# Performance work log

Hardware: AMD Instinct MI355X
Metric: run time of the kernel (lower is better)

Reference implementation:

```python
import jax, jax.numpy as jnp
import numpy as np

N_NODES = 50000
N_EDGES = 800000
IN_DIM = 3
OUT_DIM = 50


def _glorot(key, shape):
    fan_in, fan_out = shape[0], shape[1]
    lim = np.sqrt(6.0 / (fan_in + fan_out))
    return jax.random.uniform(key, shape, jnp.float32, -lim, lim)


def setup_inputs() -> dict:
    key = jax.random.key(0)
    ks = jax.random.split(key, 16)
    x = jax.random.normal(ks[0], (N_NODES, IN_DIM), jnp.float32)
    edge_index = jax.random.randint(ks[1], (2, N_EDGES), 0, N_NODES, jnp.int64)
    return {
        "x": x,
        "edge_index": edge_index,
        # pointwise Conv1d (kernel_size=1) == per-node Linear; store as [in, out]
        "w1": _glorot(ks[2], (IN_DIM, 32)), "b1": jnp.zeros((32,), jnp.float32),
        "w2": _glorot(ks[3], (32, 64)),     "b2": jnp.zeros((64,), jnp.float32),
        "w3": _glorot(ks[4], (64, 128)),    "b3": jnp.zeros((128,), jnp.float32),
        # GCNConv weights [in, out] + bias
        "g1w": _glorot(ks[5], (128, 256)),  "g1b": jnp.zeros((256,), jnp.float32),
        "g2w": _glorot(ks[6], (256, 512)),  "g2b": jnp.zeros((512,), jnp.float32),
        "g3w": _glorot(ks[7], (512, OUT_DIM)), "g3b": jnp.zeros((OUT_DIM,), jnp.float32),
    }


def _gcn_conv(h, src, dst, dinv, W, b):
    """PyG GCNConv: add self-loops + symmetric norm. h: [N, Fin]."""
    n = h.shape[0]
    h = h @ W  # [N, Fout]
    norm = dinv[src] * dinv[dst]  # [E]
    msg = h[src] * norm[:, None]  # gather over edges [E, Fout]
    agg = jax.ops.segment_sum(msg, dst, num_segments=n)
    # self-loop contribution: norm = dinv[i]^2
    agg = agg + h * (dinv * dinv)[:, None]
    return agg + b


def reference(x, edge_index, w1, b1, w2, b2, w3, b3, g1w, g1b, g2w, g2b, g3w, g3b):
    src, dst = edge_index[0], edge_index[1]
    n = x.shape[0]
    # degree with self-loops (in-degree on targets), shared by all GCN layers
    deg = jnp.zeros((n,), x.dtype).at[dst].add(1.0) + 1.0
    dinv = jax.lax.rsqrt(deg)

    # pointwise conv stack (1x1 Conv1d == per-node dense layer)
    h = jax.nn.relu(x @ w1 + b1)
    h = jax.nn.relu(h @ w2 + b2)
    h = jax.nn.relu(h @ w3 + b3)

    h = jax.nn.relu(_gcn_conv(h, src, dst, dinv, g1w, g1b))
    h = jax.nn.relu(_gcn_conv(h, src, dst, dinv, g2w, g2b))
    h = _gcn_conv(h, src, dst, dinv, g3w, g3b)
    return jax.nn.softmax(h, axis=1)  # [N, OUT_DIM]
```

## Files before the change

kernel.cpp:

```cpp
#include <hip/hip_runtime.h>
#include <hip/hip_bf16.h>
#include <math.h>


typedef __attribute__((ext_vector_type(8))) short short8;
typedef __attribute__((ext_vector_type(8))) _Float16 half8;
typedef __attribute__((ext_vector_type(4))) float floatx4;

__device__ __forceinline__ unsigned short bf16h(float f) {
    unsigned int u = __float_as_uint(f);
    u += 0x7fff + ((u >> 16) & 1);
    return (unsigned short)(u >> 16);
}
__device__ __forceinline__ float bf16f(unsigned short h) {
    return __uint_as_float(((unsigned int)h) << 16);
}

__device__ __forceinline__ void gld_lds16(unsigned short* lds, const unsigned short* g) {
    __builtin_amdgcn_global_load_lds(
        (const __attribute__((address_space(1))) unsigned int*)g,
        (__attribute__((address_space(3))) unsigned int*)lds, 16, 0, 0);
}


__global__ void hist_kernel(const int* __restrict__ dst, int* __restrict__ counts, int e) {
    int g = blockIdx.x * blockDim.x + threadIdx.x;
    if (g < e) atomicAdd(&counts[dst[g]], 1);
}

__global__ void scan1_kernel(const int* __restrict__ counts, int* __restrict__ bsum, int n) {
    __shared__ int buf[256];
    int i = blockIdx.x * 256 + threadIdx.x;
    buf[threadIdx.x] = (i < n) ? counts[i] : 0;
    __syncthreads();
    for (int off = 128; off > 0; off >>= 1) {
        if (threadIdx.x < off) buf[threadIdx.x] += buf[threadIdx.x + off];
        __syncthreads();
    }
    if (threadIdx.x == 0) bsum[blockIdx.x] = buf[0];
}

__global__ void scan2_kernel(const int* __restrict__ bsum, int* __restrict__ bsumx,
                             int* __restrict__ offsets, int nb, int n) {
    __shared__ int buf[256];
    int tid = threadIdx.x;
    int v = (tid < nb) ? bsum[tid] : 0;
    buf[tid] = v;
    __syncthreads();
    for (int off = 1; off < 256; off <<= 1) {
        int t = (tid >= off) ? buf[tid - off] : 0;
        __syncthreads();
        buf[tid] += t;
        __syncthreads();
    }
    if (tid < nb) bsumx[tid] = buf[tid] - v;
    if (tid == 255) offsets[n] = buf[255];
}

__global__ void scan3_kernel(const int* __restrict__ counts, const int* __restrict__ bsumx,
                             int* __restrict__ offsets, int* __restrict__ cursor,
                             float* __restrict__ dinv, int n) {
    __shared__ int buf[256];
    int tid = threadIdx.x;
    int i = blockIdx.x * 256 + tid;
    int c = (i < n) ? counts[i] : 0;
    buf[tid] = c;
    __syncthreads();
    for (int off = 1; off < 256; off <<= 1) {
        int t = (tid >= off) ? buf[tid - off] : 0;
        __syncthreads();
        buf[tid] += t;
        __syncthreads();
    }
    if (i < n) {
        int excl = bsumx[blockIdx.x] + buf[tid] - c;
        offsets[i] = excl;
        cursor[i] = excl;
        dinv[i] = rsqrtf((float)c + 1.0f);
    }
}

__global__ void fill_kernel(const int* __restrict__ src, const int* __restrict__ dst,
                            const float* __restrict__ dinv, int* __restrict__ cursor,
                            int* __restrict__ ssrc, float* __restrict__ snorm, int e) {
    int g = blockIdx.x * blockDim.x + threadIdx.x;
    if (g >= e) return;
    int s = src[g], d = dst[g];
    int pos = atomicAdd(&cursor[d], 1);
    ssrc[pos]  = s;
    snorm[pos] = dinv[s] * dinv[d];
}


__device__ __forceinline__ void wsplit_one(float w, unsigned short* Bt, int k, int n, int K) {
    unsigned short h = bf16h(w);
    unsigned short l = bf16h(w - bf16f(h));
    size_t base = (size_t)n * (2 * K);
    Bt[base + k]     = h;
    Bt[base + K + k] = l;
}

__global__ void prepw_kernel(const float* __restrict__ g1w, const float* __restrict__ g2w,
                             const float* __restrict__ g3w, const float* __restrict__ w3,
                             unsigned short* __restrict__ Bt1,
                             unsigned short* __restrict__ Bt2,
                             unsigned short* __restrict__ Bt3,
                             unsigned short* __restrict__ Bt0) {
    int gid = blockIdx.x * blockDim.x + threadIdx.x;
    if (gid < 32768) {
        int k = gid >> 8, n = gid & 255;
        wsplit_one(g1w[gid], Bt1, k, n, 128);
    } else if (gid < 32768 + 131072) {
        int idx = gid - 32768;
        int k = idx >> 9, n = idx & 511;
        wsplit_one(g2w[idx], Bt2, k, n, 256);
    } else if (gid < 32768 + 131072 + 32768) {
        int idx = gid - 32768 - 131072;
        int k = idx >> 6, c = idx & 63;
        float w = (c < 50) ? g3w[k * 50 + c] : 0.0f;
        wsplit_one(w, Bt3, k, c, 512);
    } else if (gid < 32768 + 131072 + 32768 + 8192) {
        int idx = gid - 32768 - 131072 - 32768;
        int k = idx >> 7, n = idx & 127;
        wsplit_one(w3[idx], Bt0, k, n, 64);
    }
}


__global__ __launch_bounds__(256) void mlp12_kernel(
        const float* __restrict__ x,
        const float* __restrict__ w1, const float* __restrict__ b1,
        const float* __restrict__ w2, const float* __restrict__ b2,
        unsigned short* __restrict__ H2h, unsigned short* __restrict__ H2l, int n) {
    __shared__ float sw1[96], sb1[32], sw2[2048], sb2[64];
    int tid = threadIdx.x;
    if (tid < 96) sw1[tid] = w1[tid];
    if (tid < 32) sb1[tid] = b1[tid];
    if (tid < 64) sb2[tid] = b2[tid];
    for (int i = tid; i < 2048; i += 256) sw2[i] = w2[i];
    __syncthreads();

    int node = blockIdx.x * 256 + tid;
    if (node >= n) return;
    float x0 = x[node * 3 + 0], x1 = x[node * 3 + 1], x2 = x[node * 3 + 2];
    float h1[32];
#pragma unroll
    for (int j = 0; j < 32; j++)
        h1[j] = fmaxf(sb1[j] + x0 * sw1[j] + x1 * sw1[32 + j] + x2 * sw1[64 + j], 0.0f);

    float acc[64];
#pragma unroll
    for (int j = 0; j < 64; j++) acc[j] = sb2[j];
    for (int k = 0; k < 32; k++) {
        float hk = h1[k];
#pragma unroll
        for (int j4 = 0; j4 < 16; j4++) {
            float4 w = *(const float4*)&sw2[k * 64 + j4 * 4];
            acc[j4 * 4 + 0] = fmaf(hk, w.x, acc[j4 * 4 + 0]);
            acc[j4 * 4 + 1] = fmaf(hk, w.y, acc[j4 * 4 + 1]);
            acc[j4 * 4 + 2] = fmaf(hk, w.z, acc[j4 * 4 + 2]);
            acc[j4 * 4 + 3] = fmaf(hk, w.w, acc[j4 * 4 + 3]);
        }
    }
#pragma unroll
    for (int j4 = 0; j4 < 16; j4++) {
        ushort4 h4, l4;
        unsigned short* hp = (unsigned short*)&h4;
        unsigned short* lp = (unsigned short*)&l4;
#pragma unroll
        for (int t = 0; t < 4; t++) {
            float v = fmaxf(acc[j4 * 4 + t], 0.0f);
            unsigned short h = bf16h(v);
            hp[t] = h;
            lp[t] = bf16h(v - bf16f(h));
        }
        *(ushort4*)&H2h[(size_t)node * 64 + j4 * 4] = h4;
        *(ushort4*)&H2l[(size_t)node * 64 + j4 * 4] = l4;
    }
}


template<int BM, int BN, int WAVES, int WGR, int WGC, int WRF, int WCF, int MODE,
         bool AF16, int SWIZCOLS>
__global__ __launch_bounds__(WAVES * 64) void gemm_mfma_kernel(
        const unsigned short* __restrict__ Ah, const unsigned short* __restrict__ Al,
        const unsigned short* __restrict__ Bt, const float* __restrict__ bias,
        float* __restrict__ Cf, unsigned short* __restrict__ Ch,
        unsigned short* __restrict__ Cl, int M, int K, int N) {
    static_assert(WGR * WRF * 16 == BM, "row cover");
    static_assert(WGC * WCF * 16 == BN, "col cover");
    static_assert(WGR * WGC == WAVES, "wave grid");
    constexpr int AUNITS = AF16 ? (BM / 16) : (BM / 8);
    constexpr int BUNITS = BN / 8;
    static_assert(AUNITS % WAVES == 0 && BUNITS % WAVES == 0, "staging split");
    __shared__ __align__(16) unsigned short Ash[BM * 32];
    __shared__ __align__(16) unsigned short Asl[AF16 ? 16 : BM * 32];
    __shared__ __align__(16) unsigned short Bsh[BN * 32];
    __shared__ __align__(16) unsigned short Bsl[BN * 32];

    int bm, bn;
    if (SWIZCOLS > 0) {
        constexpr int CSH = (SWIZCOLS == 4) ? 2 : 1;
        int b = blockIdx.x;
        int col = (b >> 3) & (SWIZCOLS - 1);
        int row = ((b >> (3 + CSH)) << 3) | (b & 7);
        bm = row * BM;
        bn = col * BN;
        if (bm >= M) return;
    } else {
        bm = blockIdx.y * BM;
        bn = blockIdx.x * BN;
    }

    const int tid  = threadIdx.x;
    const int lane = tid & 63;
    const int wave = tid >> 6;
    const int K2 = 2 * K;

    const int wr0 = (wave / WGC) * (WRF * 16);
    const int wc0 = (wave % WGC) * (WCF * 16);
    const int lr   = lane & 15;
    const int quad = lane >> 4;
    const int arow = lane >> 2;
    const int acol = (lane & 3) * 8;

    floatx4 acc[WRF][WCF];
#pragma unroll
    for (int i = 0; i < WRF; i++)
#pragma unroll
        for (int j = 0; j < WCF; j++) acc[i][j] = floatx4{0.f, 0.f, 0.f, 0.f};

    for (int k0 = 0; k0 < K; k0 += 32) {
#pragma unroll
        for (int u = 0; u < AUNITS / WAVES; u++) {
            int unit = wave + u * WAVES;
            if (AF16) {
                int grp = unit;
                int gm = bm + grp * 16 + arow;
                if (gm >= M) gm = M - 1;
                gld_lds16(&Ash[grp * 512], Ah + (size_t)gm * K + k0 + acol);
            } else {
                int grp = unit >> 1, pl = unit & 1;
                int gm = bm + grp * 16 + arow;
                if (gm >= M) gm = M - 1;
                size_t go = (size_t)gm * K + k0 + acol;
                if (pl) gld_lds16(&Asl[grp * 512], Al + go);
                else    gld_lds16(&Ash[grp * 512], Ah + go);
            }
        }
#pragma unroll
        for (int u = 0; u < BUNITS / WAVES; u++) {
            int unit = wave + u * WAVES;
            int grp = unit >> 1, pl = unit & 1;
            int gr = bn + grp * 16 + arow;
            size_t go = (size_t)gr * K2 + k0 + acol + (pl ? K : 0);
            if (pl) gld_lds16(&Bsl[grp * 512], Bt + go);
            else    gld_lds16(&Bsh[grp * 512], Bt + go);
        }
        __syncthreads();

        short8 ahf[WRF], alf[WRF], bhf[WCF], blf[WCF];
#pragma unroll
        for (int i = 0; i < WRF; i++) {
            int ro = (wr0 + i * 16 + lr) * 32 + quad * 8;
            if (AF16) {
                half8 av = *reinterpret_cast<const half8*>(&Ash[ro]);
#pragma unroll
                for (int t = 0; t < 8; t++) {
                    float f = (float)av[t];
                    unsigned short h = bf16h(f);
                    ahf[i][t] = (short)h;
                    alf[i][t] = (short)bf16h(f - bf16f(h));
                }
            } else {
                ahf[i] = *reinterpret_cast<const short8*>(&Ash[ro]);
                alf[i] = *reinterpret_cast<const short8*>(&Asl[ro]);
            }
        }
#pragma unroll
        for (int j = 0; j < WCF; j++) {
            int ro = (wc0 + j * 16 + lr) * 32 + quad * 8;
            bhf[j] = *reinterpret_cast<const short8*>(&Bsh[ro]);
            blf[j] = *reinterpret_cast<const short8*>(&Bsl[ro]);
        }
#pragma unroll
        for (int i = 0; i < WRF; i++)
#pragma unroll
            for (int j = 0; j < WCF; j++) {
                acc[i][j] = __builtin_amdgcn_mfma_f32_16x16x32_bf16(
                    ahf[i], bhf[j], acc[i][j], 0, 0, 0);
                acc[i][j] = __builtin_amdgcn_mfma_f32_16x16x32_bf16(
                    ahf[i], blf[j], acc[i][j], 0, 0, 0);
                acc[i][j] = __builtin_amdgcn_mfma_f32_16x16x32_bf16(
                    alf[i], bhf[j], acc[i][j], 0, 0, 0);
            }
        __syncthreads();
    }

#pragma unroll
    for (int i = 0; i < WRF; i++) {
#pragma unroll
        for (int j = 0; j < WCF; j++) {
            int gc = bn + wc0 + j * 16 + lr;
#pragma unroll
            for (int reg = 0; reg < 4; reg++) {
                int gr = bm + wr0 + i * 16 + quad * 4 + reg;
                if (gr >= M) continue;
                float v = acc[i][j][reg];
                if (MODE == 0) {
                    v = fmaxf(v + bias[gc], 0.0f);
                    Cf[(size_t)gr * N + gc] = v;
                } else if (MODE == 1) {
                    v = fmaxf(v + bias[gc], 0.0f);
                    unsigned short h = bf16h(v);
                    unsigned short l = bf16h(v - bf16f(h));
                    Ch[(size_t)gr * N + gc] = h;
                    Cl[(size_t)gr * N + gc] = l;
                } else if (MODE == 2) {
                    Cf[(size_t)gr * N + gc] = v;
                } else if (MODE == 3) {
                    v = fmaxf(v + bias[gc], 0.0f);
                    ((_Float16*)Ch)[(size_t)gr * N + gc] = (_Float16)v;
                } else {
                    ((_Float16*)Ch)[(size_t)gr * N + gc] = (_Float16)v;
                }
            }
        }
    }
}


template<int F>
__global__ void agg_f16_kernel(const _Float16* __restrict__ table,
                               const int* __restrict__ offsets,
                               const int* __restrict__ ssrc,
                               const float* __restrict__ snorm,
                               const float* __restrict__ dinv,
                               _Float16* __restrict__ Aout, int n) {
    constexpr int F8 = F / 8;
    int gid = blockIdx.x * blockDim.x + threadIdx.x;
    if (gid >= n * F8) return;
    int node = gid / F8;
    int c8 = (gid - node * F8) * 8;

    float acc[8];
#pragma unroll
    for (int i = 0; i < 8; i++) acc[i] = 0.0f;

    int beg = offsets[node], end = offsets[node + 1];
    for (int e = beg; e < end; ++e) {
        int s = ssrc[e];
        float w = snorm[e];
        half8 r = *reinterpret_cast<const half8*>(table + (size_t)s * F + c8);
#pragma unroll
        for (int i = 0; i < 8; i++) acc[i] = fmaf((float)r[i], w, acc[i]);
    }
    float dv = dinv[node];
    float sw = dv * dv;
    half8 r = *reinterpret_cast<const half8*>(table + (size_t)node * F + c8);
#pragma unroll
    for (int i = 0; i < 8; i++) acc[i] = fmaf((float)r[i], sw, acc[i]);

    half8 o;
#pragma unroll
    for (int i = 0; i < 8; i++) o[i] = (_Float16)acc[i];
    *reinterpret_cast<half8*>(&Aout[(size_t)node * F + c8]) = o;
}


__global__ void agg50_softmax_kernel(const _Float16* __restrict__ z,
                                     const int* __restrict__ offsets,
                                     const int* __restrict__ ssrc,
                                     const float* __restrict__ snorm,
                                     const float* __restrict__ dinv,
                                     const float* __restrict__ bias,
                                     float* __restrict__ out, int n) {
    int node = blockIdx.x * 4 + (threadIdx.x >> 6);
    int lane = threadIdx.x & 63;
    if (node >= n) return;

    float a0 = 0.f, a1 = 0.f, a2 = 0.f, a3 = 0.f;
    int beg = offsets[node], end = offsets[node + 1];
    int e = beg;
    for (; e + 4 <= end; e += 4) {
        int s0 = ssrc[e + 0], s1 = ssrc[e + 1], s2 = ssrc[e + 2], s3 = ssrc[e + 3];
        float w0 = snorm[e + 0], w1 = snorm[e + 1];
        float w2 = snorm[e + 2], w3 = snorm[e + 3];
        float r0 = (float)z[(size_t)s0 * 64 + lane];
        float r1 = (float)z[(size_t)s1 * 64 + lane];
        float r2 = (float)z[(size_t)s2 * 64 + lane];
        float r3 = (float)z[(size_t)s3 * 64 + lane];
        a0 = fmaf(r0, w0, a0);
        a1 = fmaf(r1, w1, a1);
        a2 = fmaf(r2, w2, a2);
        a3 = fmaf(r3, w3, a3);
    }
    for (; e < end; ++e)
        a0 = fmaf((float)z[(size_t)ssrc[e] * 64 + lane], snorm[e], a0);

    float dv = dinv[node];
    float a = fmaf((float)z[(size_t)node * 64 + lane], dv * dv,
                   (a0 + a1) + (a2 + a3));

    float v = (lane < 50) ? a + bias[lane] : -INFINITY;
    float m = v;
#pragma unroll
    for (int off = 32; off > 0; off >>= 1) m = fmaxf(m, __shfl_xor(m, off));
    float ex = (lane < 50) ? expf(v - m) : 0.0f;
    float s = ex;
#pragma unroll
    for (int off = 32; off > 0; off >>= 1) s += __shfl_xor(s, off);
    if (lane < 50) out[(size_t)node * 50 + lane] = ex / s;
}


extern "C" void kernel_launch(void* const* d_in, const int* in_sizes, int n_in,
                              void* d_out, int out_size, void* d_ws, size_t ws_size,
                              hipStream_t stream) {
    const float* x    = (const float*)d_in[0];
    const int*   ei   = (const int*)  d_in[1];
    const float* w1   = (const float*)d_in[2];
    const float* b1   = (const float*)d_in[3];
    const float* w2   = (const float*)d_in[4];
    const float* b2   = (const float*)d_in[5];
    const float* w3   = (const float*)d_in[6];
    const float* b3   = (const float*)d_in[7];
    const float* g1w  = (const float*)d_in[8];
    const float* g1b  = (const float*)d_in[9];
    const float* g2w  = (const float*)d_in[10];
    const float* g2b  = (const float*)d_in[11];
    const float* g3w  = (const float*)d_in[12];
    const float* g3b  = (const float*)d_in[13];
    float* out = (float*)d_out;

    const int N = in_sizes[0] / 3;
    const int E = in_sizes[1] / 2;
    const int* src = ei;
    const int* dst = ei + E;
    const int NB = (N + 255) / 256;

    char* ws = (char*)d_ws;
    size_t off = 0;
    auto alloc = [&](size_t bytes) -> char* {
        char* p = ws + off;
        off = (off + bytes + 255) & ~(size_t)255;
        return p;
    };
    int*   counts  = (int*)  alloc((size_t)N * 4);
    int*   offsets = (int*)  alloc((size_t)(N + 1) * 4);
    int*   cursor  = (int*)  alloc((size_t)N * 4);
    float* dinv    = (float*)alloc((size_t)N * 4);
    int*   bsum    = (int*)  alloc((size_t)256 * 4);
    int*   bsumx   = (int*)  alloc((size_t)256 * 4);
    int*   ssrc    = (int*)  alloc((size_t)E * 4);
    float* snorm   = (float*)alloc((size_t)E * 4);
    unsigned short* Bt1 = (unsigned short*)alloc((size_t)256 * 256 * 2);
    unsigned short* Bt2 = (unsigned short*)alloc((size_t)512 * 512 * 2);
    unsigned short* Bt3 = (unsigned short*)alloc((size_t)64 * 1024 * 2);
    unsigned short* Bt0 = (unsigned short*)alloc((size_t)128 * 128 * 2);
    char* R1 = alloc((size_t)N * 256 * 4);
    char* R2 = alloc((size_t)N * 256 * 4);
    char* R3 = alloc((size_t)N * 512 * 2);
    (void)ws_size;

    _Float16*       S128f = (_Float16*)R1;
    _Float16*       A128f = (_Float16*)(R1 + (size_t)N * 128 * 2);
    _Float16*       A256f = (_Float16*)R1;
    unsigned short* H2h  = (unsigned short*)R2;
    unsigned short* H2l  = (unsigned short*)(R2 + (size_t)N * 64 * 2);
    _Float16*       G1f  = (_Float16*)R2;
    _Float16*       zbuf = (_Float16*)R2;
    _Float16*       A512f = (_Float16*)R3;

    hipMemsetAsync(counts, 0, (size_t)N * 4, stream);
    hist_kernel<<<(E + 255) / 256, 256, 0, stream>>>(dst, counts, E);
    scan1_kernel<<<NB, 256, 0, stream>>>(counts, bsum, N);
    scan2_kernel<<<1, 256, 0, stream>>>(bsum, bsumx, offsets, NB, N);
    scan3_kernel<<<NB, 256, 0, stream>>>(counts, bsumx, offsets, cursor, dinv, N);
    fill_kernel<<<(E + 255) / 256, 256, 0, stream>>>(src, dst, dinv, cursor, ssrc, snorm, E);
    prepw_kernel<<<(204800 + 255) / 256, 256, 0, stream>>>(
        g1w, g2w, g3w, w3, Bt1, Bt2, Bt3, Bt0);

    const int MB = (N + 127) / 128;
    const int MB8 = (MB + 7) & ~7;
    const int MB64 = (N + 63) / 64;

    mlp12_kernel<<<NB, 256, 0, stream>>>(x, w1, b1, w2, b2, H2h, H2l, N);
    {   dim3 grid(1, MB);
        gemm_mfma_kernel<128, 128, 4, 2, 2, 4, 4, 3, false, 0><<<grid, 256, 0, stream>>>(
            H2h, H2l, Bt0, b3, nullptr, (unsigned short*)S128f, nullptr, N, 64, 128);
    }

    agg_f16_kernel<128><<<((size_t)N * 16 + 255) / 256, 256, 0, stream>>>(
        S128f, offsets, ssrc, snorm, dinv, A128f, N);
    {
        gemm_mfma_kernel<128, 128, 4, 2, 2, 4, 4, 3, true, 2><<<2 * MB8, 256, 0, stream>>>(
            (const unsigned short*)A128f, nullptr, Bt1, g1b,
            nullptr, (unsigned short*)G1f, nullptr, N, 128, 256);
    }

    agg_f16_kernel<256><<<((size_t)N * 32 + 255) / 256, 256, 0, stream>>>(
        G1f, offsets, ssrc, snorm, dinv, A256f, N);
    {
        gemm_mfma_kernel<128, 128, 4, 2, 2, 4, 4, 3, true, 4><<<4 * MB8, 256, 0, stream>>>(
            (const unsigned short*)A256f, nullptr, Bt2, g2b,
            nullptr, (unsigned short*)A512f, nullptr, N, 256, 512);
    }

    {   dim3 grid(1, MB64);
        gemm_mfma_kernel<64, 64, 4, 4, 1, 1, 4, 4, true, 0><<<grid, 256, 0, stream>>>(
            (const unsigned short*)A512f, nullptr, Bt3, nullptr,
            nullptr, (unsigned short*)zbuf, nullptr, N, 512, 64);
    }
    agg50_softmax_kernel<<<(N + 3) / 4, 256, 0, stream>>>(
        zbuf, offsets, ssrc, snorm, dinv, g3b, out, N);
}
```

Baseline: 489.6 us.

## Use native fp16 MFMA for first three GEMMs instead of split-bf16 emulation

```diff
diff --git a/kernel.cpp b/kernel.cpp
--- a/kernel.cpp
+++ b/kernel.cpp
@@ -92,37 +92,33 @@
 }
 
 
-__device__ __forceinline__ void wsplit_one(float w, unsigned short* Bt, int k, int n, int K) {
-    unsigned short h = bf16h(w);
-    unsigned short l = bf16h(w - bf16f(h));
-    size_t base = (size_t)n * (2 * K);
-    Bt[base + k]     = h;
-    Bt[base + K + k] = l;
-}
-
 __global__ void prepw_kernel(const float* __restrict__ g1w, const float* __restrict__ g2w,
                              const float* __restrict__ g3w, const float* __restrict__ w3,
-                             unsigned short* __restrict__ Bt1,
-                             unsigned short* __restrict__ Bt2,
+                             _Float16* __restrict__ Bt1f,
+                             _Float16* __restrict__ Bt2f,
                              unsigned short* __restrict__ Bt3,
-                             unsigned short* __restrict__ Bt0) {
+                             _Float16* __restrict__ Bt0f) {
     int gid = blockIdx.x * blockDim.x + threadIdx.x;
     if (gid < 32768) {
         int k = gid >> 8, n = gid & 255;
-        wsplit_one(g1w[gid], Bt1, k, n, 128);
+        Bt1f[(size_t)n * 128 + k] = (_Float16)g1w[gid];
     } else if (gid < 32768 + 131072) {
         int idx = gid - 32768;
         int k = idx >> 9, n = idx & 511;
-        wsplit_one(g2w[idx], Bt2, k, n, 256);
+        Bt2f[(size_t)n * 256 + k] = (_Float16)g2w[idx];
     } else if (gid < 32768 + 131072 + 32768) {
         int idx = gid - 32768 - 131072;
         int k = idx >> 6, c = idx & 63;
         float w = (c < 50) ? g3w[k * 50 + c] : 0.0f;
-        wsplit_one(w, Bt3, k, c, 512);
+        unsigned short h = bf16h(w);
+        unsigned short l = bf16h(w - bf16f(h));
+        size_t base = (size_t)c * 1024;
+        Bt3[base + k]       = h;
+        Bt3[base + 512 + k] = l;
     } else if (gid < 32768 + 131072 + 32768 + 8192) {
         int idx = gid - 32768 - 131072 - 32768;
         int k = idx >> 7, n = idx & 127;
-        wsplit_one(w3[idx], Bt0, k, n, 64);
+        Bt0f[(size_t)n * 64 + k] = (_Float16)w3[idx];
     }
 }
 
@@ -131,7 +127,7 @@
         const float* __restrict__ x,
         const float* __restrict__ w1, const float* __restrict__ b1,
         const float* __restrict__ w2, const float* __restrict__ b2,
-        unsigned short* __restrict__ H2h, unsigned short* __restrict__ H2l, int n) {
+        _Float16* __restrict__ H2f, int n) {
     __shared__ float sw1[96], sb1[32], sw2[2048], sb2[64];
     int tid = threadIdx.x;
     if (tid < 96) sw1[tid] = w1[tid];
@@ -163,40 +159,28 @@
         }
     }
 #pragma unroll
-    for (int j4 = 0; j4 < 16; j4++) {
-        ushort4 h4, l4;
-        unsigned short* hp = (unsigned short*)&h4;
-        unsigned short* lp = (unsigned short*)&l4;
-#pragma unroll
-        for (int t = 0; t < 4; t++) {
-            float v = fmaxf(acc[j4 * 4 + t], 0.0f);
-            unsigned short h = bf16h(v);
-            hp[t] = h;
-            lp[t] = bf16h(v - bf16f(h));
-        }
-        *(ushort4*)&H2h[(size_t)node * 64 + j4 * 4] = h4;
-        *(ushort4*)&H2l[(size_t)node * 64 + j4 * 4] = l4;
-    }
-}
-
-
-template<int BM, int BN, int WAVES, int WGR, int WGC, int WRF, int WCF, int MODE,
-         bool AF16, int SWIZCOLS>
-__global__ __launch_bounds__(WAVES * 64) void gemm_mfma_kernel(
-        const unsigned short* __restrict__ Ah, const unsigned short* __restrict__ Al,
-        const unsigned short* __restrict__ Bt, const float* __restrict__ bias,
-        float* __restrict__ Cf, unsigned short* __restrict__ Ch,
-        unsigned short* __restrict__ Cl, int M, int K, int N) {
+    for (int j8 = 0; j8 < 8; j8++) {
+        half8 o;
+#pragma unroll
+        for (int t = 0; t < 8; t++)
+            o[t] = (_Float16)fmaxf(acc[j8 * 8 + t], 0.0f);
+        *reinterpret_cast<half8*>(&H2f[(size_t)node * 64 + j8 * 8]) = o;
+    }
+}
+
+
+template<int BM, int BN, int WAVES, int WGR, int WGC, int WRF, int WCF, int SWIZCOLS>
+__global__ __launch_bounds__(WAVES * 64) void gemm_f16_kernel(
+        const _Float16* __restrict__ A, const _Float16* __restrict__ Btf,
+        const float* __restrict__ bias, _Float16* __restrict__ C,
+        int M, int K, int N) {
     static_assert(WGR * WRF * 16 == BM, "row cover");
     static_assert(WGC * WCF * 16 == BN, "col cover");
     static_assert(WGR * WGC == WAVES, "wave grid");
-    constexpr int AUNITS = AF16 ? (BM / 16) : (BM / 8);
-    constexpr int BUNITS = BN / 8;
+    constexpr int AUNITS = BM / 16, BUNITS = BN / 16;
     static_assert(AUNITS % WAVES == 0 && BUNITS % WAVES == 0, "staging split");
     __shared__ __align__(16) unsigned short Ash[BM * 32];
-    __shared__ __align__(16) unsigned short Asl[AF16 ? 16 : BM * 32];
     __shared__ __align__(16) unsigned short Bsh[BN * 32];
-    __shared__ __align__(16) unsigned short Bsl[BN * 32];
 
     int bm, bn;
     if (SWIZCOLS > 0) {
@@ -215,8 +199,6 @@
     const int tid  = threadIdx.x;
     const int lane = tid & 63;
     const int wave = tid >> 6;
-    const int K2 = 2 * K;
-
     const int wr0 = (wave / WGC) * (WRF * 16);
     const int wc0 = (wave % WGC) * (WCF * 16);
     const int lr   = lane & 15;
@@ -233,20 +215,96 @@
     for (int k0 = 0; k0 < K; k0 += 32) {
 #pragma unroll
         for (int u = 0; u < AUNITS / WAVES; u++) {
-            int unit = wave + u * WAVES;
-            if (AF16) {
-                int grp = unit;
-                int gm = bm + grp * 16 + arow;
-                if (gm >= M) gm = M - 1;
-                gld_lds16(&Ash[grp * 512], Ah + (size_t)gm * K + k0 + acol);
-            } else {
-                int grp = unit >> 1, pl = unit & 1;
-                int gm = bm + grp * 16 + arow;
-                if (gm >= M) gm = M - 1;
-                size_t go = (size_t)gm * K + k0 + acol;
-                if (pl) gld_lds16(&Asl[grp * 512], Al + go);
-                else    gld_lds16(&Ash[grp * 512], Ah + go);
+            int grp = wave + u * WAVES;
+            int gm = bm + grp * 16 + arow;
+            if (gm >= M) gm = M - 1;
+            gld_lds16(&Ash[grp * 512],
+                      (const unsigned short*)(A + (size_t)gm * K + k0 + acol));
+        }
+#pragma unroll
+        for (int u = 0; u < BUNITS / WAVES; u++) {
+            int grp = wave + u * WAVES;
+            int gr = bn + grp * 16 + arow;
+            gld_lds16(&Bsh[grp * 512],
+                      (const unsigned short*)(Btf + (size_t)gr * K + k0 + acol));
+        }
+        __syncthreads();
+
+        half8 af[WRF], bf[WCF];
+#pragma unroll
+        for (int i = 0; i < WRF; i++)
+            af[i] = *reinterpret_cast<const half8*>(
+                &Ash[(wr0 + i * 16 + lr) * 32 + quad * 8]);
+#pragma unroll
+        for (int j = 0; j < WCF; j++)
+            bf[j] = *reinterpret_cast<const half8*>(
+                &Bsh[(wc0 + j * 16 + lr) * 32 + quad * 8]);
+#pragma unroll
+        for (int i = 0; i < WRF; i++)
+#pragma unroll
+            for (int j = 0; j < WCF; j++)
+                acc[i][j] = __builtin_amdgcn_mfma_f32_16x16x32_f16(
+                    af[i], bf[j], acc[i][j], 0, 0, 0);
+        __syncthreads();
+    }
+
+#pragma unroll
+    for (int i = 0; i < WRF; i++) {
+#pragma unroll
+        for (int j = 0; j < WCF; j++) {
+            int gc = bn + wc0 + j * 16 + lr;
+#pragma unroll
+            for (int reg = 0; reg < 4; reg++) {
+                int gr = bm + wr0 + i * 16 + quad * 4 + reg;
+                if (gr >= M) continue;
+                float v = fmaxf(acc[i][j][reg] + bias[gc], 0.0f);
+                C[(size_t)gr * N + gc] = (_Float16)v;
             }
+        }
+    }
+}
+
+
+template<int BM, int BN, int WAVES, int WGR, int WGC, int WRF, int WCF>
+__global__ __launch_bounds__(WAVES * 64) void gemm_emul_kernel(
+        const _Float16* __restrict__ Af, const unsigned short* __restrict__ Bt,
+        _Float16* __restrict__ C, int M, int K, int N) {
+    static_assert(WGR * WRF * 16 == BM, "row cover");
+    static_assert(WGC * WCF * 16 == BN, "col cover");
+    static_assert(WGR * WGC == WAVES, "wave grid");
+    constexpr int AUNITS = BM / 16, BUNITS = BN / 8;
+    static_assert(AUNITS % WAVES == 0 && BUNITS % WAVES == 0, "staging split");
+    __shared__ __align__(16) unsigned short Ash[BM * 32];
+    __shared__ __align__(16) unsigned short Bsh[BN * 32];
+    __shared__ __align__(16) unsigned short Bsl[BN * 32];
+
+    const int bm = blockIdx.y * BM;
+    const int bn = blockIdx.x * BN;
+    const int tid  = threadIdx.x;
+    const int lane = tid & 63;
+    const int wave = tid >> 6;
+    const int K2 = 2 * K;
+    const int wr0 = (wave / WGC) * (WRF * 16);
+    const int wc0 = (wave % WGC) * (WCF * 16);
+    const int lr   = lane & 15;
+    const int quad = lane >> 4;
+    const int arow = lane >> 2;
+    const int acol = (lane & 3) * 8;
+
+    floatx4 acc[WRF][WCF];
+#pragma unroll
+    for (int i = 0; i < WRF; i++)
+#pragma unroll
+        for (int j = 0; j < WCF; j++) acc[i][j] = floatx4{0.f, 0.f, 0.f, 0.f};
+
+    for (int k0 = 0; k0 < K; k0 += 32) {
+#pragma unroll
+        for (int u = 0; u < AUNITS / WAVES; u++) {
+            int grp = wave + u * WAVES;
+            int gm = bm + grp * 16 + arow;
+            if (gm >= M) gm = M - 1;
+            gld_lds16(&Ash[grp * 512],
+                      (const unsigned short*)(Af + (size_t)gm * K + k0 + acol));
         }
 #pragma unroll
         for (int u = 0; u < BUNITS / WAVES; u++) {
@@ -262,19 +320,14 @@
         short8 ahf[WRF], alf[WRF], bhf[WCF], blf[WCF];
 #pragma unroll
         for (int i = 0; i < WRF; i++) {
-            int ro = (wr0 + i * 16 + lr) * 32 + quad * 8;
-            if (AF16) {
-                half8 av = *reinterpret_cast<const half8*>(&Ash[ro]);
-#pragma unroll
-                for (int t = 0; t < 8; t++) {
-                    float f = (float)av[t];
-                    unsigned short h = bf16h(f);
-                    ahf[i][t] = (short)h;
-                    alf[i][t] = (short)bf16h(f - bf16f(h));
-                }
-            } else {
-                ahf[i] = *reinterpret_cast<const short8*>(&Ash[ro]);
-                alf[i] = *reinterpret_cast<const short8*>(&Asl[ro]);
+            half8 av = *reinterpret_cast<const half8*>(
+                &Ash[(wr0 + i * 16 + lr) * 32 + quad * 8]);
+#pragma unroll
+            for (int t = 0; t < 8; t++) {
+                float f = (float)av[t];
+                unsigned short h = bf16h(f);
+                ahf[i][t] = (short)h;
+                alf[i][t] = (short)bf16h(f - bf16f(h));
             }
         }
 #pragma unroll
@@ -306,24 +359,7 @@
             for (int reg = 0; reg < 4; reg++) {
                 int gr = bm + wr0 + i * 16 + quad * 4 + reg;
                 if (gr >= M) continue;
-                float v = acc[i][j][reg];
-                if (MODE == 0) {
-                    v = fmaxf(v + bias[gc], 0.0f);
-                    Cf[(size_t)gr * N + gc] = v;
-                } else if (MODE == 1) {
-                    v = fmaxf(v + bias[gc], 0.0f);
-                    unsigned short h = bf16h(v);
-                    unsigned short l = bf16h(v - bf16f(h));
-                    Ch[(size_t)gr * N + gc] = h;
-                    Cl[(size_t)gr * N + gc] = l;
-                } else if (MODE == 2) {
-                    Cf[(size_t)gr * N + gc] = v;
-                } else if (MODE == 3) {
-                    v = fmaxf(v + bias[gc], 0.0f);
-                    ((_Float16*)Ch)[(size_t)gr * N + gc] = (_Float16)v;
-                } else {
-                    ((_Float16*)Ch)[(size_t)gr * N + gc] = (_Float16)v;
-                }
+                C[(size_t)gr * N + gc] = (_Float16)acc[i][j][reg];
             }
         }
     }
@@ -454,10 +490,10 @@
     int*   bsumx   = (int*)  alloc((size_t)256 * 4);
     int*   ssrc    = (int*)  alloc((size_t)E * 4);
     float* snorm   = (float*)alloc((size_t)E * 4);
-    unsigned short* Bt1 = (unsigned short*)alloc((size_t)256 * 256 * 2);
-    unsigned short* Bt2 = (unsigned short*)alloc((size_t)512 * 512 * 2);
+    _Float16* Bt1f = (_Float16*)alloc((size_t)256 * 128 * 2);
+    _Float16* Bt2f = (_Float16*)alloc((size_t)512 * 256 * 2);
     unsigned short* Bt3 = (unsigned short*)alloc((size_t)64 * 1024 * 2);
-    unsigned short* Bt0 = (unsigned short*)alloc((size_t)128 * 128 * 2);
+    _Float16* Bt0f = (_Float16*)alloc((size_t)128 * 64 * 2);
     char* R1 = alloc((size_t)N * 256 * 4);
     char* R2 = alloc((size_t)N * 256 * 4);
     char* R3 = alloc((size_t)N * 512 * 2);
@@ -466,8 +502,7 @@
     _Float16*       S128f = (_Float16*)R1;
     _Float16*       A128f = (_Float16*)(R1 + (size_t)N * 128 * 2);
     _Float16*       A256f = (_Float16*)R1;
-    unsigned short* H2h  = (unsigned short*)R2;
-    unsigned short* H2l  = (unsigned short*)(R2 + (size_t)N * 64 * 2);
+    _Float16*       H2f  = (_Float16*)R2;
     _Float16*       G1f  = (_Float16*)R2;
     _Float16*       zbuf = (_Float16*)R2;
     _Float16*       A512f = (_Float16*)R3;
@@ -479,38 +514,31 @@
     scan3_kernel<<<NB, 256, 0, stream>>>(counts, bsumx, offsets, cursor, dinv, N);
     fill_kernel<<<(E + 255) / 256, 256, 0, stream>>>(src, dst, dinv, cursor, ssrc, snorm, E);
     prepw_kernel<<<(204800 + 255) / 256, 256, 0, stream>>>(
-        g1w, g2w, g3w, w3, Bt1, Bt2, Bt3, Bt0);
+        g1w, g2w, g3w, w3, Bt1f, Bt2f, Bt3, Bt0f);
 
     const int MB = (N + 127) / 128;
     const int MB8 = (MB + 7) & ~7;
     const int MB64 = (N + 63) / 64;
 
-    mlp12_kernel<<<NB, 256, 0, stream>>>(x, w1, b1, w2, b2, H2h, H2l, N);
+    mlp12_kernel<<<NB, 256, 0, stream>>>(x, w1, b1, w2, b2, H2f, N);
     {   dim3 grid(1, MB);
-        gemm_mfma_kernel<128, 128, 4, 2, 2, 4, 4, 3, false, 0><<<grid, 256, 0, stream>>>(
-            H2h, H2l, Bt0, b3, nullptr, (unsigned short*)S128f, nullptr, N, 64, 128);
+        gemm_f16_kernel<128, 128, 4, 2, 2, 4, 4, 0><<<grid, 256, 0, stream>>>(
+            H2f, Bt0f, b3, S128f, N, 64, 128);
     }
 
     agg_f16_kernel<128><<<((size_t)N * 16 + 255) / 256, 256, 0, stream>>>(
         S128f, offsets, ssrc, snorm, dinv, A128f, N);
-    {
-        gemm_mfma_kernel<128, 128, 4, 2, 2, 4, 4, 3, true, 2><<<2 * MB8, 256, 0, stream>>>(
-            (const unsigned short*)A128f, nullptr, Bt1, g1b,
-            nullptr, (unsigned short*)G1f, nullptr, N, 128, 256);
-    }
+    gemm_f16_kernel<128, 128, 4, 2, 2, 4, 4, 2><<<2 * MB8, 256, 0, stream>>>(
+        A128f, Bt1f, g1b, G1f, N, 128, 256);
 
     agg_f16_kernel<256><<<((size_t)N * 32 + 255) / 256, 256, 0, stream>>>(
         G1f, offsets, ssrc, snorm, dinv, A256f, N);
-    {
-        gemm_mfma_kernel<128, 128, 4, 2, 2, 4, 4, 3, true, 4><<<4 * MB8, 256, 0, stream>>>(
-            (const unsigned short*)A256f, nullptr, Bt2, g2b,
-            nullptr, (unsigned short*)A512f, nullptr, N, 256, 512);
-    }
+    gemm_f16_kernel<128, 128, 4, 2, 2, 4, 4, 4><<<4 * MB8, 256, 0, stream>>>(
+        A256f, Bt2f, g2b, A512f, N, 256, 512);
 
     {   dim3 grid(1, MB64);
-        gemm_mfma_kernel<64, 64, 4, 4, 1, 1, 4, 4, true, 0><<<grid, 256, 0, stream>>>(
-            (const unsigned short*)A512f, nullptr, Bt3, nullptr,
-            nullptr, (unsigned short*)zbuf, nullptr, N, 512, 64);
+        gemm_emul_kernel<64, 64, 4, 4, 1, 1, 4><<<grid, 256, 0, stream>>>(
+            A512f, Bt3, zbuf, N, 512, 64);
     }
     agg50_softmax_kernel<<<(N + 3) / 4, 256, 0, stream>>>(
         zbuf, offsets, ssrc, snorm, dinv, g3b, out, N);
```

Result: faster. 453.9 us (-7.3%).
